# Kernel optimization log

Measured on AMD Instinct MI355X. Metric: run time of the kernel, lower is better.

## Reference

```python
import jax, jax.numpy as jnp
import numpy as np

DIM = 384
HEADS = 12
WIN = (7, 7)
N = WIN[0] * WIN[1]  # 49 tokens per window
B = 2048             # total windows
NW = 64              # windows per image (mask groups)


def _relative_position_index():
    ch, cw = np.meshgrid(np.arange(WIN[0]), np.arange(WIN[1]), indexing='ij')
    coords = np.stack([ch, cw]).reshape(2, -1)                 # [2, N]
    rel = coords[:, :, None] - coords[:, None, :]              # [2, N, N]
    rel = rel.transpose(1, 2, 0)                               # [N, N, 2]
    rel[..., 0] += WIN[0] - 1
    rel[..., 1] += WIN[1] - 1
    rel[..., 0] *= 2 * WIN[1] - 1
    return rel.sum(-1).astype(np.int32)                        # [N, N]


def setup_inputs() -> dict:
    key = jax.random.key(0)
    ks = jax.random.split(key, 7)
    table_sz = (2 * WIN[0] - 1) * (2 * WIN[1] - 1)             # 169
    return {
        'x': jax.random.normal(ks[0], (B, N, DIM), jnp.float32),
        'mask': jax.random.normal(ks[1], (NW, N, N), jnp.float32),
        'qkv_w': jax.random.normal(ks[2], (3 * DIM, DIM), jnp.float32) * (DIM ** -0.5),
        'qkv_b': jnp.zeros((3 * DIM,), jnp.float32),
        'proj_w': jax.random.normal(ks[3], (DIM, DIM), jnp.float32) * (DIM ** -0.5),
        'proj_b': jnp.zeros((DIM,), jnp.float32),
        'rel_table': jax.random.normal(ks[4], (table_sz, HEADS), jnp.float32) * 0.02,
        'rel_index': jnp.asarray(_relative_position_index()),
    }


def reference(x, mask, qkv_w, qkv_b, proj_w, proj_b, rel_table, rel_index):
    b, n, c = x.shape
    h, hd = HEADS, c // HEADS
    scale = hd ** -0.5
    qkv = (x @ qkv_w.T + qkv_b).reshape(b, n, 3, h, hd)
    q, k, v = (qkv[:, :, 0].transpose(0, 2, 1, 3),
               qkv[:, :, 1].transpose(0, 2, 1, 3),
               qkv[:, :, 2].transpose(0, 2, 1, 3))             # [b, h, n, hd]
    attn = jnp.einsum('bhid,bhjd->bhij', q * scale, k)         # [b, h, n, n]
    bias = rel_table[rel_index.reshape(-1)].reshape(n, n, h).transpose(2, 0, 1)
    attn = attn + bias[None]
    nw = mask.shape[0]
    attn = attn.reshape(b // nw, nw, h, n, n) + mask[None, :, None]
    attn = jax.nn.softmax(attn.reshape(b, h, n, n), axis=-1)
    out = jnp.einsum('bhij,bhjd->bihd', attn, v).reshape(b, n, c)
    return out @ proj_w.T + proj_b
```

## Files before the change

### kernel.cpp

```cpp
#include <hip/hip_runtime.h>

#define DIM   384
#define HEADS 12
#define NTOK  49
#define NWIN  2048
#define NMASK 64
#define HD    32
#define MTOT  (NWIN * NTOK)

typedef __bf16 bf16x8 __attribute__((ext_vector_type(8)));
typedef float  floatx4 __attribute__((ext_vector_type(4)));

__device__ __forceinline__ unsigned short f2bf(float f) {
  unsigned int u = __builtin_bit_cast(unsigned int, f);
  u += 0x7fffu + ((u >> 16) & 1u);
  return (unsigned short)(u >> 16);
}
__device__ __forceinline__ void async_copy16(const void* g, void* l) {
  __builtin_amdgcn_global_load_lds((const __attribute__((address_space(1))) void*)g,
                                   (__attribute__((address_space(3))) void*)l, 16, 0, 0);
}

__global__ void prep_kernel(const float* __restrict__ x,
                            const float* __restrict__ qkv_w,
                            const float* __restrict__ proj_w,
                            const float* __restrict__ rel_table,
                            const int*   __restrict__ rel_index,
                            const float* __restrict__ mask,
                            unsigned short* __restrict__ xb,
                            unsigned short* __restrict__ qkv_wb,
                            unsigned short* __restrict__ proj_wb,
                            float* __restrict__ biasP,
                            float* __restrict__ maskP) {
  const int tid  = blockIdx.x * blockDim.x + threadIdx.x;
  const int nthr = gridDim.x * blockDim.x;

  const int nx4 = (MTOT * DIM) / 4;
  for (int i = tid; i < nx4; i += nthr) {
    float4 v = ((const float4*)x)[i];
    ushort4 o = { f2bf(v.x), f2bf(v.y), f2bf(v.z), f2bf(v.w) };
    ((ushort4*)xb)[i] = o;
  }
  const int nw4 = (3 * DIM * DIM) / 4;
  for (int i = tid; i < nw4; i += nthr) {
    float4 v = ((const float4*)qkv_w)[i];
    ushort4 o = { f2bf(v.x), f2bf(v.y), f2bf(v.z), f2bf(v.w) };
    ((ushort4*)qkv_wb)[i] = o;
  }
  const int np4 = (DIM * DIM) / 4;
  for (int i = tid; i < np4; i += nthr) {
    float4 v = ((const float4*)proj_w)[i];
    ushort4 o = { f2bf(v.x), f2bf(v.y), f2bf(v.z), f2bf(v.w) };
    ((ushort4*)proj_wb)[i] = o;
  }
  for (int i = tid; i < 12288; i += nthr) {
    const int lane = i & 63;
    const int t    = (i >> 6) & 15;
    const int h    = i >> 10;
    const int rb   = (t >> 2) * 16 + (lane >> 4) * 4;
    const int c    = (t & 3) * 16 + (lane & 15);
    float4 o;
    float* op = (float*)&o;
#pragma unroll
    for (int reg = 0; reg < 4; reg++) {
      const int r = rb + reg;
      op[reg] = (r < NTOK && c < NTOK)
                  ? rel_table[rel_index[r * NTOK + c] * HEADS + h]
                  : -1e30f;
    }
    ((float4*)biasP)[i] = o;
  }
  for (int i = tid; i < 65536; i += nthr) {
    const int lane = i & 63;
    const int t    = (i >> 6) & 15;
    const int g    = i >> 10;
    const int rb   = (t >> 2) * 16 + (lane >> 4) * 4;
    const int c    = (t & 3) * 16 + (lane & 15);
    float4 o;
    float* op = (float*)&o;
#pragma unroll
    for (int reg = 0; reg < 4; reg++) {
      const int r = rb + reg;
      op[reg] = (r < NTOK && c < NTOK)
                  ? mask[g * (NTOK * NTOK) + r * NTOK + c]
                  : -1e30f;
    }
    ((float4*)maskP)[i] = o;
  }
}

template <int OUT_BF16>
__global__ __launch_bounds__(256, 2)
void gemm_bt(const unsigned short* __restrict__ A,
             const unsigned short* __restrict__ W,
             const float* __restrict__ bias,
             void* __restrict__ Cout,
             int M, int N, int K) {
  constexpr int ESTR = OUT_BF16 ? 144 : 272;
  constexpr int ESZ  = 16 * ESTR;
  __shared__ __align__(16) char lds[OUT_BF16 ? (4 * 2 * 16 * 144)
                                             : (4 * 2 * 16 * 272)];
  char* ldsA = lds;
  char* ldsB = lds + 8192;

  const int tid  = threadIdx.x;
  const int lane = tid & 63;
  const int wave = tid >> 6;
  const int wr   = wave >> 1;
  const int wc   = wave & 1;
  const int q4   = lane >> 4;
  const int lm   = lane & 15;

  const int NT  = N >> 7;
  const int cpx = gridDim.x >> 3;
  const int lin = (blockIdx.x & 7) * cpx + (blockIdx.x >> 3);
  const int tileM = (lin / NT) * 128;
  const int tileN = (lin % NT) * 128;

  const int srow = tid >> 2;
  const int scol = (tid & 3) * 8;
  const unsigned short* gA = A + (size_t)(tileM + srow) * K + scol;
  const unsigned short* gB = W + (size_t)(tileN + srow) * K + scol;
  const int loff = tid * 16;

  const int aoff = (wr * 64 + lm) * 64 + q4 * 16;
  const int boff = (wc * 64 + lm) * 64 + q4 * 16;

  floatx4 acc[4][4] = {};

  for (int k0 = 0; k0 < K; k0 += 32) {
    async_copy16(gA,          ldsA + loff);
    async_copy16(gA + 64 * K, ldsA + 4096 + loff);
    async_copy16(gB,          ldsB + loff);
    async_copy16(gB + 64 * K, ldsB + 4096 + loff);
    gA += 32; gB += 32;
    __syncthreads();

    bf16x8 af[4], bfr[4];
#pragma unroll
    for (int i = 0; i < 4; i++) {
      af[i]  = *(const bf16x8*)(ldsA + aoff + i * 1024);
      bfr[i] = *(const bf16x8*)(ldsB + boff + i * 1024);
    }
#pragma unroll
    for (int i = 0; i < 4; i++)
#pragma unroll
      for (int j = 0; j < 4; j++)
        acc[i][j] = __builtin_amdgcn_mfma_f32_16x16x32_bf16(af[i], bfr[j], acc[i][j], 0, 0, 0);
    __syncthreads();
  }

  float bvj[4];
#pragma unroll
  for (int j = 0; j < 4; j++) bvj[j] = bias[tileN + wc * 64 + j * 16 + lm];

  char* Eb = lds + wave * (2 * ESZ);
#pragma unroll
  for (int i = 0; i < 4; i++) {
    char* Ep = Eb + (i & 1) * ESZ;
    if (OUT_BF16) {
#pragma unroll
      for (int j = 0; j < 4; j++)
#pragma unroll
        for (int r = 0; r < 4; r++)
          *(unsigned short*)(Ep + (q4 * 4 + r) * 144 + (j * 16 + lm) * 2) =
              f2bf(acc[i][j][r] + bvj[j]);
#pragma unroll
      for (int it = 0; it < 2; it++) {
        const int c   = lane + it * 64;
        const int row = c >> 3;
        const int c8  = c & 7;
        const uint4 v = *(const uint4*)(Ep + row * 144 + c8 * 16);
        unsigned short* dst = (unsigned short*)Cout +
            (size_t)(tileM + wr * 64 + i * 16 + row) * N + tileN + wc * 64 + c8 * 8;
        *(uint4*)dst = v;
      }
    } else {
#pragma unroll
      for (int j = 0; j < 4; j++)
#pragma unroll
        for (int r = 0; r < 4; r++)
          *(float*)(Ep + (q4 * 4 + r) * 272 + (j * 16 + lm) * 4) =
              acc[i][j][r] + bvj[j];
#pragma unroll
      for (int it = 0; it < 4; it++) {
        const int c   = lane + it * 64;
        const int row = c >> 4;
        const int c4  = c & 15;
        const uint4 v = *(const uint4*)(Ep + row * 272 + c4 * 16);
        float* dst = (float*)Cout +
            (size_t)(tileM + wr * 64 + i * 16 + row) * N + tileN + wc * 64 + c4 * 4;
        *(uint4*)dst = v;
      }
    }
  }
}

__global__ __launch_bounds__(256, 8)
void attn_mfma(const unsigned short* __restrict__ qkv,
               const float* __restrict__ biasP,
               const float* __restrict__ maskP,
               unsigned short* __restrict__ attn_out) {
  __shared__ __align__(16) char lds[16128];
  char* Vt = lds;
  char* Qb = lds + 6912;
  char* Kb = lds + 11008;
  char* Pb = lds + 6912;

  const int tid  = threadIdx.x;
  const int wave = tid >> 6;
  const int lane = tid & 63;
  const int lm   = lane & 15;
  const int q    = lane >> 4;

  const int pair = (blockIdx.x & 7) * (NWIN * HEADS / 8) + (blockIdx.x >> 3);
  const int b    = pair / HEADS;
  const int h    = pair - b * HEADS;
  const int g    = b & (NMASK - 1);

  const unsigned short* qbase = qkv + (size_t)b * NTOK * (3 * DIM) + h * HD;

  {
    const int row   = tid >> 2;
    const int chunk = tid & 3;
    uint4 vq = {0u, 0u, 0u, 0u}, vk = vq;
    if (row < NTOK) {
      vq = *(const uint4*)(qbase + (size_t)row * (3 * DIM) + chunk * 8);
      vk = *(const uint4*)(qbase + (size_t)row * (3 * DIM) + DIM + chunk * 8);
    }
    *(uint4*)(Qb + row * 64 + chunk * 16) = vq;
    *(uint4*)(Kb + row * 64 + chunk * 16) = vk;
  }
  {
    const int tok = tid >> 2;
    const int c   = tid & 3;
    uint4 vv = {0u, 0u, 0u, 0u};
    if (tok < NTOK) vv = *(const uint4*)(qbase + 2 * DIM + (size_t)tok * (3 * DIM) + c * 8);
    const unsigned short* e = (const unsigned short*)&vv;
#pragma unroll
    for (int j = 0; j < 8; j++)
      *(unsigned short*)(Vt + (c * 8 + j) * 144 + tok * 2) = e[j];
    if (tid < 64)
      *(unsigned short*)(Vt + HD * 144 + tid * 2) =
          (tid < NTOK) ? (unsigned short)0x3F80 : (unsigned short)0;
  }
  __syncthreads();

  bf16x8 qf, kf[4];
  qf = *(const bf16x8*)(Qb + (wave * 16 + lm) * 64 + q * 16);
#pragma unroll
  for (int j = 0; j < 4; j++)
    kf[j] = *(const bf16x8*)(Kb + (j * 16 + lm) * 64 + q * 16);
  floatx4 S[4] = {};
#pragma unroll
  for (int j = 0; j < 4; j++)
    S[j] = __builtin_amdgcn_mfma_f32_16x16x32_bf16(qf, kf[j], S[j], 0, 0, 0);

  __syncthreads();

  const float scale = 0.17677669529663687f;
  const float* bb = biasP + (size_t)h * 4096;
  const float* mm = maskP + (size_t)g * 4096;
#pragma unroll
  for (int j = 0; j < 4; j++) {
    const int t = wave * 4 + j;
    const float4 b4 = ((const float4*)bb)[t * 64 + lane];
    const float4 m4 = ((const float4*)mm)[t * 64 + lane];
    const float* bp = (const float*)&b4;
    const float* mp = (const float*)&m4;
#pragma unroll
    for (int r = 0; r < 4; r++) {
      const float s = fmaf(S[j][r], scale, bp[r] + mp[r]);
      const float p = __expf(s);
      *(unsigned short*)(Pb + (wave * 16 + q * 4 + r) * 144 + (j * 16 + lm) * 2) = f2bf(p);
    }
  }

  floatx4 O[3] = {};
#pragma unroll
  for (int ks = 0; ks < 2; ks++) {
    const bf16x8 pf = *(const bf16x8*)(Pb + (wave * 16 + lm) * 144 + ks * 64 + q * 16);
#pragma unroll
    for (int n = 0; n < 3; n++) {
      const bf16x8 vf = *(const bf16x8*)(Vt + (n * 16 + lm) * 144 + ks * 64 + q * 16);
      O[n] = __builtin_amdgcn_mfma_f32_16x16x32_bf16(pf, vf, O[n], 0, 0, 0);
    }
  }

  unsigned short* obase = attn_out + (size_t)b * NTOK * DIM + h * HD;
#pragma unroll
  for (int r = 0; r < 4; r++) {
    const float sv  = __shfl(O[2][r], lane & 48, 64);
    const float inv = __builtin_amdgcn_rcpf(sv);
    const int row = wave * 16 + q * 4 + r;
    if (row < NTOK) {
#pragma unroll
      for (int n = 0; n < 2; n++)
        obase[(size_t)row * DIM + n * 16 + lm] = f2bf(O[n][r] * inv);
    }
  }
}

extern "C" void kernel_launch(void* const* d_in, const int* in_sizes, int n_in,
                              void* d_out, int out_size, void* d_ws, size_t ws_size,
                              hipStream_t stream) {
  const float* x         = (const float*)d_in[0];
  const float* mask      = (const float*)d_in[1];
  const float* qkv_w     = (const float*)d_in[2];
  const float* qkv_b     = (const float*)d_in[3];
  const float* proj_w    = (const float*)d_in[4];
  const float* proj_b    = (const float*)d_in[5];
  const float* rel_table = (const float*)d_in[6];
  const int*   rel_index = (const int*)d_in[7];
  float* out = (float*)d_out;

  char* ws = (char*)d_ws;
  unsigned short* xb      = (unsigned short*)(ws);
  unsigned short* qkvbuf  = (unsigned short*)(ws + 77070336);
  unsigned short* qkv_wb  = (unsigned short*)(ws + 308281344);
  unsigned short* proj_wb = (unsigned short*)(ws + 309166080);
  float*          biasP   = (float*)(ws + 309460992);
  float*          maskP   = (float*)(ws + 309657600);

  prep_kernel<<<2048, 256, 0, stream>>>(x, qkv_w, proj_w, rel_table, rel_index,
                                        mask, xb, qkv_wb, proj_wb, biasP, maskP);

  gemm_bt<1><<<dim3((MTOT / 128) * ((3 * DIM) / 128)), 256, 0, stream>>>(
      xb, qkv_wb, qkv_b, qkvbuf, MTOT, 3 * DIM, DIM);

  attn_mfma<<<dim3(NWIN * HEADS), 256, 0, stream>>>(qkvbuf, biasP, maskP,
                                                    xb );

  gemm_bt<0><<<dim3((MTOT / 128) * (DIM / 128)), 256, 0, stream>>>(
      xb , proj_wb, proj_b, out, MTOT, DIM, DIM);
}
```

Measured before the change: 546.4 us.

## Fuse fp32-to-bf16 conversion of x into the QKV GEMM A-tile loads

Removes the separate pass that converted x to bf16 in the prep kernel. The QKV GEMM now reads fp32 x directly, converts it in registers, and stores bf16 into LDS, prefetching the next K-slice into registers. This avoids a full read and write of the activation tensor. In exchange, A tiles are re-read as fp32 across N-tiles, and the async LDS copy is replaced by register-staged stores.

```diff
diff --git a/kernel.cpp b/kernel.cpp
--- a/kernel.cpp
+++ b/kernel.cpp
@@ -16,18 +16,24 @@
   u += 0x7fffu + ((u >> 16) & 1u);
   return (unsigned short)(u >> 16);
 }
+__device__ __forceinline__ uint4 cvt8(float4 a, float4 b) {
+  uint4 r;
+  r.x = (unsigned)f2bf(a.x) | ((unsigned)f2bf(a.y) << 16);
+  r.y = (unsigned)f2bf(a.z) | ((unsigned)f2bf(a.w) << 16);
+  r.z = (unsigned)f2bf(b.x) | ((unsigned)f2bf(b.y) << 16);
+  r.w = (unsigned)f2bf(b.z) | ((unsigned)f2bf(b.w) << 16);
+  return r;
+}
 __device__ __forceinline__ void async_copy16(const void* g, void* l) {
   __builtin_amdgcn_global_load_lds((const __attribute__((address_space(1))) void*)g,
                                    (__attribute__((address_space(3))) void*)l, 16, 0, 0);
 }
 
-__global__ void prep_kernel(const float* __restrict__ x,
-                            const float* __restrict__ qkv_w,
+__global__ void prep_kernel(const float* __restrict__ qkv_w,
                             const float* __restrict__ proj_w,
                             const float* __restrict__ rel_table,
                             const int*   __restrict__ rel_index,
                             const float* __restrict__ mask,
-                            unsigned short* __restrict__ xb,
                             unsigned short* __restrict__ qkv_wb,
                             unsigned short* __restrict__ proj_wb,
                             float* __restrict__ biasP,
@@ -35,12 +41,6 @@
   const int tid  = blockIdx.x * blockDim.x + threadIdx.x;
   const int nthr = gridDim.x * blockDim.x;
 
-  const int nx4 = (MTOT * DIM) / 4;
-  for (int i = tid; i < nx4; i += nthr) {
-    float4 v = ((const float4*)x)[i];
-    ushort4 o = { f2bf(v.x), f2bf(v.y), f2bf(v.z), f2bf(v.w) };
-    ((ushort4*)xb)[i] = o;
-  }
   const int nw4 = (3 * DIM * DIM) / 4;
   for (int i = tid; i < nw4; i += nthr) {
     float4 v = ((const float4*)qkv_w)[i];
@@ -89,9 +89,9 @@
   }
 }
 
-template <int OUT_BF16>
+template <int OUT_BF16, int A_FP32>
 __global__ __launch_bounds__(256, 2)
-void gemm_bt(const unsigned short* __restrict__ A,
+void gemm_bt(const void* __restrict__ Ap,
              const unsigned short* __restrict__ W,
              const float* __restrict__ bias,
              void* __restrict__ Cout,
@@ -119,22 +119,52 @@
 
   const int srow = tid >> 2;
   const int scol = (tid & 3) * 8;
-  const unsigned short* gA = A + (size_t)(tileM + srow) * K + scol;
+  const unsigned short* gA = nullptr;
+  const float*          gAf = nullptr;
+  if constexpr (A_FP32)
+    gAf = (const float*)Ap + (size_t)(tileM + srow) * K + scol;
+  else
+    gA = (const unsigned short*)Ap + (size_t)(tileM + srow) * K + scol;
   const unsigned short* gB = W + (size_t)(tileN + srow) * K + scol;
   const int loff = tid * 16;
 
   const int aoff = (wr * 64 + lm) * 64 + q4 * 16;
   const int boff = (wc * 64 + lm) * 64 + q4 * 16;
 
+  float4 pa0, pa1, pa2, pa3;
+  if constexpr (A_FP32) {
+    pa0 = *(const float4*)(gAf);
+    pa1 = *(const float4*)(gAf + 4);
+    pa2 = *(const float4*)(gAf + (size_t)64 * K);
+    pa3 = *(const float4*)(gAf + (size_t)64 * K + 4);
+    gAf += 32;
+  }
+
   floatx4 acc[4][4] = {};
 
   for (int k0 = 0; k0 < K; k0 += 32) {
-    async_copy16(gA,          ldsA + loff);
-    async_copy16(gA + 64 * K, ldsA + 4096 + loff);
+    if constexpr (A_FP32) {
+      *(uint4*)(ldsA + loff)        = cvt8(pa0, pa1);
+      *(uint4*)(ldsA + 4096 + loff) = cvt8(pa2, pa3);
+    } else {
+      async_copy16(gA,          ldsA + loff);
+      async_copy16(gA + 64 * K, ldsA + 4096 + loff);
+      gA += 32;
+    }
     async_copy16(gB,          ldsB + loff);
     async_copy16(gB + 64 * K, ldsB + 4096 + loff);
-    gA += 32; gB += 32;
+    gB += 32;
     __syncthreads();
+
+    if constexpr (A_FP32) {
+      if (k0 + 32 < K) {
+        pa0 = *(const float4*)(gAf);
+        pa1 = *(const float4*)(gAf + 4);
+        pa2 = *(const float4*)(gAf + (size_t)64 * K);
+        pa3 = *(const float4*)(gAf + (size_t)64 * K + 4);
+        gAf += 32;
+      }
+    }
 
     bf16x8 af[4], bfr[4];
 #pragma unroll
@@ -315,22 +345,22 @@
   float* out = (float*)d_out;
 
   char* ws = (char*)d_ws;
-  unsigned short* xb      = (unsigned short*)(ws);
+  unsigned short* attn_o  = (unsigned short*)(ws);
   unsigned short* qkvbuf  = (unsigned short*)(ws + 77070336);
   unsigned short* qkv_wb  = (unsigned short*)(ws + 308281344);
   unsigned short* proj_wb = (unsigned short*)(ws + 309166080);
   float*          biasP   = (float*)(ws + 309460992);
   float*          maskP   = (float*)(ws + 309657600);
 
-  prep_kernel<<<2048, 256, 0, stream>>>(x, qkv_w, proj_w, rel_table, rel_index,
-                                        mask, xb, qkv_wb, proj_wb, biasP, maskP);
-
-  gemm_bt<1><<<dim3((MTOT / 128) * ((3 * DIM) / 128)), 256, 0, stream>>>(
-      xb, qkv_wb, qkv_b, qkvbuf, MTOT, 3 * DIM, DIM);
+  prep_kernel<<<768, 256, 0, stream>>>(qkv_w, proj_w, rel_table, rel_index,
+                                       mask, qkv_wb, proj_wb, biasP, maskP);
+
+  gemm_bt<1, 1><<<dim3((MTOT / 128) * ((3 * DIM) / 128)), 256, 0, stream>>>(
+      x, qkv_wb, qkv_b, qkvbuf, MTOT, 3 * DIM, DIM);
 
   attn_mfma<<<dim3(NWIN * HEADS), 256, 0, stream>>>(qkvbuf, biasP, maskP,
-                                                    xb );
-
-  gemm_bt<0><<<dim3((MTOT / 128) * (DIM / 128)), 256, 0, stream>>>(
-      xb , proj_wb, proj_b, out, MTOT, DIM, DIM);
-}
+                                                    attn_o);
+
+  gemm_bt<0, 0><<<dim3((MTOT / 128) * (DIM / 128)), 256, 0, stream>>>(
+      attn_o, proj_wb, proj_b, out, MTOT, DIM, DIM);
+}
```

After: 542.6 us. No clear change (-0.7%).
